# Performance work log

Hardware: AMD Instinct MI355X
Metric: run time of the kernel (lower is better)

## Reference

```python
import jax, jax.numpy as jnp
import numpy as np


def normalize_adj(adj):
    """Symmetrize (adj + adj.T*(adj.T>adj) - adj*(adj.T>adj)), add self loops, row-normalize D^-1 A."""
    at = jnp.swapaxes(adj, -1, -2)
    mask = (at > adj).astype(adj.dtype)
    a = adj + at * mask - adj * mask
    m = a.shape[-1]
    a = a + jnp.eye(m, dtype=a.dtype)
    rowsum = a.sum(axis=-1, keepdims=True)
    inv = jnp.where(rowsum > 0, 1.0 / rowsum, 0.0)
    return a * inv


def setup_inputs() -> dict:
    key = jax.random.key(0)
    ks = jax.random.split(key, 8)
    N, n, T, dim, M = 4, 3, 512, 2048, 256
    x = jax.random.normal(ks[0], (N, n, T, dim), dtype=jnp.float32)
    nodes = jax.random.normal(ks[1], (N, M, dim), dtype=jnp.float32)
    adj = (jax.random.uniform(ks[2], (N, M, M)) < 0.05).astype(jnp.float32)
    conv_w = jax.random.normal(ks[3], (2048, dim, 3), dtype=jnp.float32) * 0.02  # OIH
    conv_b = jnp.zeros((2048,), dtype=jnp.float32)
    W1 = jax.random.normal(ks[4], (dim, dim), dtype=jnp.float32) * 0.02
    b1 = jnp.zeros((dim,), dtype=jnp.float32)
    W2 = jax.random.normal(ks[5], (dim, dim), dtype=jnp.float32) * 0.02
    b2 = jnp.zeros((dim,), dtype=jnp.float32)
    return {"x": x, "nodes": nodes, "adj": adj, "conv_w": conv_w, "conv_b": conv_b,
            "W1": W1, "b1": b1, "W2": W2, "b2": b2}


def reference(x, nodes, adj, conv_w, conv_b, W1, b1, W2, b2):
    N, n, T, dim = x.shape
    # Conv1d front-end: (N*n, C=dim, T), kernel 3, pad 1, then ReLU
    feats = x.reshape(N * n, T, dim).transpose(0, 2, 1)  # [B, C, T]
    feats = jax.lax.conv_general_dilated(
        feats, conv_w, window_strides=(1,), padding=[(1, 1)],
        dimension_numbers=("NCH", "OIH", "NCH"))
    feats = jax.nn.relu(feats + conv_b[None, :, None])
    feats = feats.transpose(0, 2, 1).reshape(N, n, T, dim)
    # GCN_Module over per-sample node graphs (batched over N)
    a = normalize_adj(adj)                                   # [N, M, M]
    h = jax.nn.relu(jnp.einsum("bij,bjf->bif", a, nodes @ W1) + b1)
    out = jnp.einsum("bij,bjf->bif", a, h @ W2) + b2         # [N, M, dim]
    return feats, out
```

## Files before the change

### kernel.cpp

```cpp
#include <hip/hip_runtime.h>
#include <stdint.h>

typedef __bf16 bf16x8 __attribute__((ext_vector_type(8)));
typedef float floatx4 __attribute__((ext_vector_type(4)));

__device__ __forceinline__ void gload_lds16(const void* g, void* l) {
    __builtin_amdgcn_global_load_lds((const __attribute__((address_space(1))) void*)g,
                                     (__attribute__((address_space(3))) void*)l, 16, 0, 0);
}

__device__ __forceinline__ uint16_t f2bf(float f) {
    uint32_t u = __float_as_uint(f);
    u += 0x7fff + ((u >> 16) & 1);
    return (uint16_t)(u >> 16);
}
__device__ __forceinline__ uint32_t f2bf2(float lo, float hi) {
    return (uint32_t)f2bf(lo) | ((uint32_t)f2bf(hi) << 16);
}

struct AmulSM {
    float vv[256];
    int   jj[256];
    float part[4];
    int   wcnt[4];
    int   woff[4];
    float sinv;
    int   n0;
};

__device__ __forceinline__ void amul_body(const float* __restrict__ adj,
                                          const float* __restrict__ H,
                                          uint16_t* __restrict__ outp,
                                          int b, int i, int tid, AmulSM* sm)
{
    const float* A = adj + ((size_t)b << 16);
    float aij = A[(i << 8) + tid];
    float aji = A[(tid << 8) + i];
    float v = fmaxf(aij, aji);
    if (tid == i) v += 1.0f;

    float s = v;
    #pragma unroll
    for (int off = 32; off > 0; off >>= 1) s += __shfl_down(s, off);

    bool pred = v != 0.0f;
    unsigned long long m = __ballot(pred);
    int wid = tid >> 6;
    if ((tid & 63) == 0) { sm->part[wid] = s; sm->wcnt[wid] = (int)__popcll(m); }
    __syncthreads();
    if (tid == 0) {
        float t = sm->part[0] + sm->part[1] + sm->part[2] + sm->part[3];
        sm->sinv = t > 0.0f ? 1.0f / t : 0.0f;
        int o = 0;
        #pragma unroll
        for (int w = 0; w < 4; ++w) { sm->woff[w] = o; o += sm->wcnt[w]; }
        sm->n0 = o;
    }
    __syncthreads();
    if (pred) {
        int pos = sm->woff[wid] + (int)__popcll(m & ((1ull << (tid & 63)) - 1ull));
        sm->vv[pos] = v * sm->sinv;
        sm->jj[pos] = tid;
    }
    __syncthreads();

    const int n0 = sm->n0;
    const int f0 = tid * 8;
    const float* Hb = H + (((size_t)b) << 8) * 2048;
    float acc[8] = {};
    for (int c = 0; c < n0; ++c) {
        float av = sm->vv[c];
        const float* hp = Hb + (size_t)sm->jj[c] * 2048 + f0;
        float4 p = *(const float4*)hp;
        float4 q = *(const float4*)(hp + 4);
        acc[0] += av * p.x; acc[1] += av * p.y; acc[2] += av * p.z; acc[3] += av * p.w;
        acc[4] += av * q.x; acc[5] += av * q.y; acc[6] += av * q.z; acc[7] += av * q.w;
    }
    uint4 o;
    o.x = f2bf2(acc[0], acc[1]);
    o.y = f2bf2(acc[2], acc[3]);
    o.z = f2bf2(acc[4], acc[5]);
    o.w = f2bf2(acc[6], acc[7]);
    *(uint4*)(outp + (((size_t)b << 8) + i) * 2048 + f0) = o;
}

__device__ __forceinline__ void amul_swizzle(int bid, int& b, int& i) {
    int x = bid & 7, g = bid >> 3;
    b = x >> 1;
    i = ((x & 1) << 7) + g;
}

#define PR_AM 1024
#define PR_W  3072
#define PR_T  5120
#define PR_N  17456

__global__ __launch_bounds__(256)
void k_prep(const float* __restrict__ x, uint16_t* __restrict__ xpad,
            const float* __restrict__ w, uint16_t* __restrict__ wT,
            const float* __restrict__ W1, const float* __restrict__ W2,
            uint16_t* __restrict__ W1T, uint16_t* __restrict__ W2T,
            const float* __restrict__ adj, const float* __restrict__ nodes,
            uint16_t* __restrict__ gbf)
{
    __shared__ union {
        float  wbuf[6144];
        float  tile[64][65];
        AmulSM am;
    } sm;
    const int bid = blockIdx.x;
    const int tid = threadIdx.x;

    if (bid < PR_AM) {
        int b, i; amul_swizzle(bid, b, i);
        amul_body(adj, nodes, gbf, b, i, tid, &sm.am);
    } else if (bid < PR_W) {
        int o = bid - PR_AM;
        const float* src = w + (size_t)o * 6144;
        uint16_t*    dst = wT + (size_t)o * 6144;
        #pragma unroll
        for (int it = 0; it < 24; ++it)
            sm.wbuf[it * 256 + tid] = src[it * 256 + tid];
        __syncthreads();
        #pragma unroll
        for (int h = 0; h < 3; ++h)
            #pragma unroll
            for (int c = 0; c < 8; ++c) {
                int i = c * 256 + tid;
                dst[h * 2048 + i] = f2bf(sm.wbuf[i * 3 + h]);
            }
    } else if (bid < PR_T) {
        int t  = bid - PR_W;
        int z  = t >> 10;
        int by = (t >> 5) & 31;
        int bx = t & 31;
        const float* src = z ? W2 : W1;
        uint16_t*    dst = z ? W2T : W1T;
        int tx = tid & 63, ty = tid >> 6;
        for (int rr = ty; rr < 64; rr += 4)
            sm.tile[rr][tx] = src[(size_t)(by * 64 + rr) * 2048 + bx * 64 + tx];
        __syncthreads();
        for (int rr = ty; rr < 64; rr += 4)
            dst[(size_t)(bx * 64 + rr) * 2048 + by * 64 + tx] = f2bf(sm.tile[tx][rr]);
    } else {
        int idx4 = (bid - PR_T) * 256 + tid;
        int ch4  = idx4 & 511;
        int tmp  = idx4 >> 9;
        int b    = tmp / 514;
        int tt   = tmp - b * 514;
        float4 v = {0.0f, 0.0f, 0.0f, 0.0f};
        if (tt >= 1 && tt <= 512)
            v = *(const float4*)(x + ((size_t)(b * 512 + tt - 1) << 11) + ch4 * 4);
        uint2 o = { f2bf2(v.x, v.y), f2bf2(v.z, v.w) };
        ((uint2*)xpad)[idx4] = o;
    }
}

template<bool RELU>
__device__ __forceinline__ void g64_tile(uint16_t* As, uint16_t* Bs,
                                         const uint16_t* __restrict__ A,
                                         const uint16_t* __restrict__ BT,
                                         float* __restrict__ C, const float* __restrict__ bias,
                                         int rt, int ct)
{
    const int tid  = threadIdx.x;
    const int lane = tid & 63;
    const int wave = tid >> 6;
    const int wm   = (wave >> 1) * 32;
    const int wn   = (wave & 1) * 32;
    const int lm   = lane & 15;
    const int kq   = (lane >> 4) * 8;
    const int sr   = tid >> 2;
    const int sc   = (tid & 3) * 8;

    const size_t abase = (size_t)(rt + sr) * 2048 + sc;
    const size_t bbase = (size_t)(ct + sr) * 2048 + sc;

    floatx4 acc[2][2] = {};

    for (int k0 = 0; k0 < 2048; k0 += 64) {
        #pragma unroll
        for (int p = 0; p < 2; ++p) {
            gload_lds16(A  + abase + k0 + p * 32, &As[p * 2048 + tid * 8]);
            gload_lds16(BT + bbase + k0 + p * 32, &Bs[p * 2048 + tid * 8]);
        }
        __syncthreads();

        #pragma unroll
        for (int s = 0; s < 2; ++s) {
            bf16x8 af[2], bfr[2];
            #pragma unroll
            for (int mt = 0; mt < 2; ++mt)
                af[mt] = *(const bf16x8*)&As[s * 2048 + (wm + mt * 16 + lm) * 32 + kq];
            #pragma unroll
            for (int nt = 0; nt < 2; ++nt)
                bfr[nt] = *(const bf16x8*)&Bs[s * 2048 + (wn + nt * 16 + lm) * 32 + kq];
            #pragma unroll
            for (int mt = 0; mt < 2; ++mt)
                #pragma unroll
                for (int nt = 0; nt < 2; ++nt)
                    acc[mt][nt] = __builtin_amdgcn_mfma_f32_16x16x32_bf16(af[mt], bfr[nt], acc[mt][nt], 0, 0, 0);
        }
        __syncthreads();
    }

    const int lq = lane >> 4;
    #pragma unroll
    for (int mt = 0; mt < 2; ++mt)
        #pragma unroll
        for (int nt = 0; nt < 2; ++nt) {
            int col = ct + wn + nt * 16 + lm;
            float bv = bias[col];
            #pragma unroll
            for (int r = 0; r < 4; ++r) {
                int row = rt + wm + mt * 16 + lq * 4 + r;
                float v = acc[mt][nt][r] + bv;
                if (RELU) v = fmaxf(v, 0.0f);
                C[(size_t)row * 2048 + col] = v;
            }
        }
}

__global__ __launch_bounds__(256)
void k_big(const uint16_t* __restrict__ xpad, const uint16_t* __restrict__ wmT,
           float* __restrict__ feats, const float* __restrict__ conv_b,
           const uint16_t* __restrict__ gbf, const uint16_t* __restrict__ W1T,
           float* __restrict__ h, const float* __restrict__ b1)
{
    __shared__ __align__(16) uint16_t lds[16384];
    const int bid  = blockIdx.x;
    const int tid  = threadIdx.x;
    const int lane = tid & 63;
    const int wave = tid >> 6;
    const int lm   = lane & 15;
    const int kq   = (lane >> 4) * 8;
    const int lq   = lane >> 4;

    if (bid < 768) {
        uint16_t* As = lds;
        uint16_t* Bs = lds + 8192;
        const int xc = bid & 7;
        const int g  = bid >> 3;
        const int rt = (12 * (xc >> 1) + (g % 12)) * 128;
        const int ct = (8 * (xc & 1) + (g / 12)) * 128;
        const int wm = (wave >> 1) * 64;
        const int wn = (wave & 1) * 64;

        const int sr = tid >> 2;
        const int sc = (tid & 3) * 8;
        size_t arow[2]; size_t brow[2];
        #pragma unroll
        for (int rh = 0; rh < 2; ++rh) {
            int r = rt + rh * 64 + sr;
            int b = r >> 9;
            int t = r & 511;
            arow[rh] = ((size_t)(b * 514 + t) << 11);
            brow[rh] = (size_t)(ct + rh * 64 + sr) * 6144;
        }

        floatx4 acc[4][4] = {};

        for (int k0 = 0; k0 < 6144; k0 += 64) {
            const int hh = k0 >> 11;
            const int icb = (k0 & 2047) + sc;
            #pragma unroll
            for (int p = 0; p < 4; ++p) {
                const int s  = p >> 1;
                const int rh = p & 1;
                gload_lds16(xpad + arow[rh] + ((size_t)hh << 11) + icb + s * 32,
                            &As[p * 2048 + tid * 8]);
                gload_lds16(wmT + brow[rh] + k0 + sc + s * 32,
                            &Bs[p * 2048 + tid * 8]);
            }
            __syncthreads();

            #pragma unroll
            for (int s = 0; s < 2; ++s) {
                bf16x8 af[4], bfr[4];
                #pragma unroll
                for (int mt = 0; mt < 4; ++mt)
                    af[mt] = *(const bf16x8*)&As[s * 4096 + (wm + mt * 16 + lm) * 32 + kq];
                #pragma unroll
                for (int nt = 0; nt < 4; ++nt)
                    bfr[nt] = *(const bf16x8*)&Bs[s * 4096 + (wn + nt * 16 + lm) * 32 + kq];
                #pragma unroll
                for (int mt = 0; mt < 4; ++mt)
                    #pragma unroll
                    for (int nt = 0; nt < 4; ++nt)
                        acc[mt][nt] = __builtin_amdgcn_mfma_f32_16x16x32_bf16(af[mt], bfr[nt], acc[mt][nt], 0, 0, 0);
            }
            __syncthreads();
        }

        #pragma unroll
        for (int mt = 0; mt < 4; ++mt)
            #pragma unroll
            for (int nt = 0; nt < 4; ++nt) {
                int col = ct + wn + nt * 16 + lm;
                float bv = conv_b[col];
                #pragma unroll
                for (int r = 0; r < 4; ++r) {
                    int row = rt + wm + mt * 16 + lq * 4 + r;
                    feats[(size_t)row * 2048 + col] = fmaxf(acc[mt][nt][r] + bv, 0.0f);
                }
            }
    } else {
        const int t  = bid - 768;
        const int xc = t & 7;
        const int g  = t >> 3;
        const int rt = (g & 15) * 64;
        const int ct = (4 * xc + (g >> 4)) * 64;
        g64_tile<true>(lds, lds + 4096, gbf, W1T, h, b1, rt, ct);
    }
}

__global__ __launch_bounds__(256)
void k_amul(const float* __restrict__ adj, const float* __restrict__ H,
            uint16_t* __restrict__ outp)
{
    __shared__ AmulSM sm;
    int b, i; amul_swizzle(blockIdx.x, b, i);
    amul_body(adj, H, outp, b, i, threadIdx.x, &sm);
}

__global__ __launch_bounds__(256)
void k_gemm64(const uint16_t* __restrict__ A, const uint16_t* __restrict__ BT,
              float* __restrict__ C, const float* __restrict__ bias)
{
    __shared__ __align__(16) uint16_t lds[8192];
    const int bid = blockIdx.x;
    const int xc  = bid & 7;
    const int g   = bid >> 3;
    const int rt  = (g & 15) * 64;
    const int ct  = (4 * xc + (g >> 4)) * 64;
    g64_tile<false>(lds, lds + 4096, A, BT, C, bias, rt, ct);
}


extern "C" void kernel_launch(void* const* d_in, const int* in_sizes, int n_in,
                              void* d_out, int out_size, void* d_ws, size_t ws_size,
                              hipStream_t stream)
{
    const float* x      = (const float*)d_in[0];
    const float* nodes  = (const float*)d_in[1];
    const float* adj    = (const float*)d_in[2];
    const float* conv_w = (const float*)d_in[3];
    const float* conv_b = (const float*)d_in[4];
    const float* W1     = (const float*)d_in[5];
    const float* b1     = (const float*)d_in[6];
    const float* W2     = (const float*)d_in[7];
    const float* b2     = (const float*)d_in[8];
    float* out = (float*)d_out;

    char* ws = (char*)d_ws;
    uint16_t* xpad   = (uint16_t*)(ws);
    uint16_t* wmT    = (uint16_t*)(ws + 25288704);
    uint16_t* W1T    = (uint16_t*)(ws + 50454528);
    uint16_t* W2T    = (uint16_t*)(ws + 58843136);
    uint16_t* gbf    = (uint16_t*)(ws + 67231744);
    float*    h      = (float*)   (ws + 71426048);
    uint16_t* ahb    = (uint16_t*)(ws + 79814656);

    k_prep<<<PR_N, 256, 0, stream>>>(x, xpad, conv_w, wmT,
                                     W1, W2, W1T, W2T, adj, nodes, gbf);
    k_big<<<1280, 256, 0, stream>>>(xpad, wmT, out, conv_b, gbf, W1T, h, b1);
    k_amul<<<1024, 256, 0, stream>>>(adj, h, ahb);
    k_gemm64<<<512, 256, 0, stream>>>(ahb, W2T, out + 12582912, b2);
}
```

Measured before the change: 411.9 us.

## Fuse GCN adjacency multiply and second GEMM into k_big with atomic counters

Folds the separate adjacency-multiply and second-GEMM kernels into the GCN branch of k_big. Per-batch and per-row-tile atomic counters, with release/acquire fences, order the h → A·h → out chain inside one launch. This removes two kernel launches and their drain gaps, and lets the GCN chain overlap with the tail of the conv GEMM blocks. In exchange, waiting blocks spin and hold CU slots. Progress relies on the producing blocks being dispatched and resident, which carries a deadlock risk if occupancy is insufficient.

```diff
diff --git a/kernel.cpp b/kernel.cpp
--- a/kernel.cpp
+++ b/kernel.cpp
@@ -16,6 +16,19 @@
 }
 __device__ __forceinline__ uint32_t f2bf2(float lo, float hi) {
     return (uint32_t)f2bf(lo) | ((uint32_t)f2bf(hi) << 16);
+}
+
+__device__ __forceinline__ void bump(int* p) {
+    __syncthreads();
+    if (threadIdx.x == 0)
+        __hip_atomic_fetch_add(p, 1, __ATOMIC_RELEASE, __HIP_MEMORY_SCOPE_AGENT);
+}
+__device__ __forceinline__ void wait_acq(int* p, int target) {
+    if (threadIdx.x == 0)
+        while (__hip_atomic_load(p, __ATOMIC_RELAXED, __HIP_MEMORY_SCOPE_AGENT) < target)
+            __builtin_amdgcn_s_sleep(16);
+    __syncthreads();
+    __builtin_amdgcn_fence(__ATOMIC_ACQUIRE, "agent");
 }
 
 struct AmulSM {
@@ -84,8 +97,8 @@
     *(uint4*)(outp + (((size_t)b << 8) + i) * 2048 + f0) = o;
 }
 
-__device__ __forceinline__ void amul_swizzle(int bid, int& b, int& i) {
-    int x = bid & 7, g = bid >> 3;
+__device__ __forceinline__ void amul_swizzle(int id, int& b, int& i) {
+    int x = id & 7, g = id >> 3;
     b = x >> 1;
     i = ((x & 1) << 7) + g;
 }
@@ -225,9 +238,16 @@
 void k_big(const uint16_t* __restrict__ xpad, const uint16_t* __restrict__ wmT,
            float* __restrict__ feats, const float* __restrict__ conv_b,
            const uint16_t* __restrict__ gbf, const uint16_t* __restrict__ W1T,
-           float* __restrict__ h, const float* __restrict__ b1)
-{
-    __shared__ __align__(16) uint16_t lds[16384];
+           float* __restrict__ h, const float* __restrict__ b1,
+           const float* __restrict__ adj, uint16_t* __restrict__ ahb,
+           const uint16_t* __restrict__ W2T, float* __restrict__ out2,
+           const float* __restrict__ b2, int* __restrict__ cntH,
+           int* __restrict__ cnt2)
+{
+    __shared__ __align__(16) union {
+        uint16_t u16[16384];
+        AmulSM   am;
+    } sm;
     const int bid  = blockIdx.x;
     const int tid  = threadIdx.x;
     const int lane = tid & 63;
@@ -237,8 +257,8 @@
     const int lq   = lane >> 4;
 
     if (bid < 768) {
-        uint16_t* As = lds;
-        uint16_t* Bs = lds + 8192;
+        uint16_t* As = sm.u16;
+        uint16_t* Bs = sm.u16 + 8192;
         const int xc = bid & 7;
         const int g  = bid >> 3;
         const int rt = (12 * (xc >> 1) + (g % 12)) * 128;
@@ -310,30 +330,22 @@
         const int g  = t >> 3;
         const int rt = (g & 15) * 64;
         const int ct = (4 * xc + (g >> 4)) * 64;
-        g64_tile<true>(lds, lds + 4096, gbf, W1T, h, b1, rt, ct);
-    }
-}
-
-__global__ __launch_bounds__(256)
-void k_amul(const float* __restrict__ adj, const float* __restrict__ H,
-            uint16_t* __restrict__ outp)
-{
-    __shared__ AmulSM sm;
-    int b, i; amul_swizzle(blockIdx.x, b, i);
-    amul_body(adj, H, outp, b, i, threadIdx.x, &sm);
-}
-
-__global__ __launch_bounds__(256)
-void k_gemm64(const uint16_t* __restrict__ A, const uint16_t* __restrict__ BT,
-              float* __restrict__ C, const float* __restrict__ bias)
-{
-    __shared__ __align__(16) uint16_t lds[8192];
-    const int bid = blockIdx.x;
-    const int xc  = bid & 7;
-    const int g   = bid >> 3;
-    const int rt  = (g & 15) * 64;
-    const int ct  = (4 * xc + (g >> 4)) * 64;
-    g64_tile<false>(lds, lds + 4096, A, BT, C, bias, rt, ct);
+
+        g64_tile<true>(sm.u16, sm.u16 + 4096, gbf, W1T, h, b1, rt, ct);
+        bump(&cntH[(g & 15) >> 2]);
+
+        int b0, i0, b1i, i1;
+        amul_swizzle(2 * t,     b0,  i0);
+        amul_swizzle(2 * t + 1, b1i, i1);
+        wait_acq(&cntH[b0], 128);
+        amul_body(adj, h, ahb, b0, i0, tid, &sm.am);
+        bump(&cnt2[b0 * 4 + (i0 >> 6)]);
+        amul_body(adj, h, ahb, b1i, i1, tid, &sm.am);
+        bump(&cnt2[b1i * 4 + (i1 >> 6)]);
+
+        wait_acq(&cnt2[g & 15], 64);
+        g64_tile<false>(sm.u16, sm.u16 + 4096, ahb, W2T, out2, b2, rt, ct);
+    }
 }
 
 
@@ -360,10 +372,12 @@
     uint16_t* gbf    = (uint16_t*)(ws + 67231744);
     float*    h      = (float*)   (ws + 71426048);
     uint16_t* ahb    = (uint16_t*)(ws + 79814656);
-
+    int*      cnt    = (int*)     (ws + 84008960);
+
+    hipMemsetAsync(cnt, 0, 128, stream);
     k_prep<<<PR_N, 256, 0, stream>>>(x, xpad, conv_w, wmT,
                                      W1, W2, W1T, W2T, adj, nodes, gbf);
-    k_big<<<1280, 256, 0, stream>>>(xpad, wmT, out, conv_b, gbf, W1T, h, b1);
-    k_amul<<<1024, 256, 0, stream>>>(adj, h, ahb);
-    k_gemm64<<<512, 256, 0, stream>>>(ahb, W2T, out + 12582912, b2);
-}
+    k_big<<<1280, 256, 0, stream>>>(xpad, wmT, out, conv_b, gbf, W1T, h, b1,
+                                    adj, ahb, W2T, out + 12582912, b2,
+                                    cnt, cnt + 4);
+}
```

After: 606.1 us. 47.1% more time.
